# Kernel tuning notes

Hardware: AMD Instinct MI355X
Metric: run time of the kernel (lower is better)

The kernel has to match this reference:

```python
import jax, jax.numpy as jnp
import numpy as np

N_NODES = 100_000
N_EDGES = 1_600_000
N_GRAPHS = 512
NF = 64        # n_node_feats
H1 = 128       # hidden width
H2 = 64        # dim_node_emb
DIM_OUT = 1
STEPS = 4      # set2set processing steps


def _lin(x, W, b):
    # torch Linear convention: y = x @ W.T + b, W: [out, in]
    return x @ W.T + b


def _gelu(x):
    return jax.nn.gelu(x, approximate=False)  # torch.nn.GELU default (erf)


def _lstm_cell(x, h, c, Wih, Whh, bih, bhh):
    g = x @ Wih.T + bih + h @ Whh.T + bhh
    i, f, gg, o = jnp.split(g, 4, axis=-1)  # torch gate order: i, f, g, o
    i, f, o = jax.nn.sigmoid(i), jax.nn.sigmoid(f), jax.nn.sigmoid(o)
    gg = jnp.tanh(gg)
    c = f * c + i * gg
    h = o * jnp.tanh(c)
    return h, c


def setup_inputs() -> dict:
    key = jax.random.key(0)
    ks = jax.random.split(key, 24)
    p = lambda k, shp: jax.random.normal(k, shp, dtype=jnp.float32) * 0.05
    inp = {
        "x": jax.random.normal(ks[0], (N_NODES, NF), dtype=jnp.float32),
        "edge_index": jax.random.randint(ks[1], (2, N_EDGES), 0, N_NODES, dtype=jnp.int32),
        "batch": jnp.sort(jax.random.randint(ks[2], (N_NODES,), 0, N_GRAPHS, dtype=jnp.int32)),
        "nfc_W": p(ks[3], (H1, NF)), "nfc_b": p(ks[4], (H1,)),
        "gc1_W": p(ks[5], (H1, H1)), "gc1_b": p(ks[6], (H1,)),
        "gc2_W": p(ks[7], (H2, H1)), "gc2_b": p(ks[8], (H2,)),
        "lstm0_Wih": p(ks[9], (4 * H2, 2 * H2)), "lstm0_Whh": p(ks[10], (4 * H2, H2)),
        "lstm0_bih": p(ks[11], (4 * H2,)), "lstm0_bhh": p(ks[12], (4 * H2,)),
        "lstm1_Wih": p(ks[13], (4 * H2, H2)), "lstm1_Whh": p(ks[14], (4 * H2, H2)),
        "lstm1_bih": p(ks[15], (4 * H2,)), "lstm1_bhh": p(ks[16], (4 * H2,)),
        "fc1_W": p(ks[17], (32, 2 * H2)), "fc1_b": p(ks[18], (32,)),
        "fc2_W": p(ks[19], (DIM_OUT, 32)), "fc2_b": p(ks[20], (DIM_OUT,)),
    }
    return inp


def _forward(x, edge_index, batch, nfc_W, nfc_b, gc1_W, gc1_b, gc2_W, gc2_b,
             lstm0_Wih, lstm0_Whh, lstm0_bih, lstm0_bhh,
             lstm1_Wih, lstm1_Whh, lstm1_bih, lstm1_bhh,
             fc1_W, fc1_b, fc2_W, fc2_b):
    src, dst = edge_index[0], edge_index[1]

    def gin_conv(h, W, b):
        # PyG GINConv, eps=0: lin((1+eps)*x + sum_{j in N(i)} x_j)
        agg = jax.ops.segment_sum(h[src], dst, num_segments=N_NODES)
        return _lin(h + agg, W, b)

    h = _gelu(_lin(x, nfc_W, nfc_b))
    h = _gelu(gin_conv(h, gc1_W, gc1_b))
    h = _gelu(gin_conv(h, gc2_W, gc2_b))
    # F.normalize(p=2, dim=1)
    h = h / jnp.maximum(jnp.linalg.norm(h, axis=1, keepdims=True), 1e-12)

    # Set2Set: 2-layer LSTM, 4 processing steps, scatter-softmax attention
    B = N_GRAPHS
    h0 = jnp.zeros((B, H2), jnp.float32); c0 = jnp.zeros((B, H2), jnp.float32)
    h1 = jnp.zeros((B, H2), jnp.float32); c1 = jnp.zeros((B, H2), jnp.float32)
    q_star = jnp.zeros((B, 2 * H2), jnp.float32)
    for _ in range(STEPS):
        h0, c0 = _lstm_cell(q_star, h0, c0, lstm0_Wih, lstm0_Whh, lstm0_bih, lstm0_bhh)
        h1, c1 = _lstm_cell(h0, h1, c1, lstm1_Wih, lstm1_Whh, lstm1_bih, lstm1_bhh)
        q = h1  # [B, H2]
        e = jnp.sum(h * q[batch], axis=-1, keepdims=True)  # [N, 1]
        m = jax.ops.segment_max(e, batch, num_segments=B)
        ex = jnp.exp(e - m[batch])
        s = jax.ops.segment_sum(ex, batch, num_segments=B)
        a = ex / (s[batch] + 1e-16)
        r = jax.ops.segment_sum(a * h, batch, num_segments=B)  # [B, H2]
        q_star = jnp.concatenate([q, r], axis=-1)

    z = _gelu(_lin(q_star, fc1_W, fc1_b))
    z = _lin(z, fc2_W, fc2_b)
    return z, h


def reference(x, edge_index, batch, nfc_W, nfc_b, gc1_W, gc1_b, gc2_W, gc2_b,
              lstm0_Wih, lstm0_Whh, lstm0_bih, lstm0_bhh,
              lstm1_Wih, lstm1_Whh, lstm1_bih, lstm1_bhh,
              fc1_W, fc1_b, fc2_W, fc2_b):
    return _forward(x, edge_index, batch, nfc_W, nfc_b, gc1_W, gc1_b, gc2_W, gc2_b,
                    lstm0_Wih, lstm0_Whh, lstm0_bih, lstm0_bhh,
                    lstm1_Wih, lstm1_Whh, lstm1_bih, lstm1_bhh,
                    fc1_W, fc1_b, fc2_W, fc2_b)
```

## Files before the change

### kernel.cpp

```cpp
#include <hip/hip_runtime.h>
#include <hip/hip_bf16.h>
#include <math.h>

constexpr int N  = 100000;
constexpr int E  = 1600000;
constexpr int NG = 512;
constexpr int NF = 64;
constexpr int H1 = 128;
constexpr int H2 = 64;

constexpr int BW   = 256;
constexpr int NB   = (N + BW - 1) / BW;
constexpr int CAP  = 4864;
constexpr int CHUNK = 8192;

constexpr int MAXN = 416;
constexpr int RST  = 68;

typedef __attribute__((ext_vector_type(8))) short short8;
typedef __attribute__((ext_vector_type(4))) float f32x4;

__device__ __forceinline__ float gelu_f(float x) {
    return 0.5f * x * (1.0f + erff(x * 0.70710678118654752f));
}
__device__ __forceinline__ float sigmoid_f(float x) {
    return 1.0f / (1.0f + expf(-x));
}
__device__ __forceinline__ float waveAllSum(float v) {
    #pragma unroll
    for (int m = 32; m; m >>= 1) v += __shfl_xor(v, m);
    return v;
}
__device__ __forceinline__ unsigned short f2bf(float x) {
    __hip_bfloat16 b = __float2bfloat16(x);
    return *reinterpret_cast<unsigned short*>(&b);
}
__device__ __forceinline__ float bf2f(unsigned short u) {
    return __uint_as_float(((unsigned int)u) << 16);
}
__device__ __forceinline__ float bf_lo(unsigned int u) { return __uint_as_float(u << 16); }
__device__ __forceinline__ float bf_hi(unsigned int u) { return __uint_as_float(u & 0xffff0000u); }

__device__ __forceinline__ void bfsplit(float v, unsigned short& hi, unsigned short& lo) {
    hi = f2bf(v);
    lo = f2bf(v - bf2f(hi));
}

__global__ __launch_bounds__(256) void bcur_init_kernel(int* __restrict__ bcursor) {
    int b = blockIdx.x * 256 + threadIdx.x;
    if (b < NB) bcursor[b] = b * CAP;
}

__global__ __launch_bounds__(256) void bin_scatter_kernel(const int* __restrict__ ei,
                                                          int* __restrict__ bcursor,
                                                          int2* __restrict__ pairs) {
    __shared__ int hist[NB];
    __shared__ int start_s[NB];
    __shared__ int lcur[NB];
    int tid = threadIdx.x;
    int e0 = blockIdx.x * CHUNK;
    for (int b = tid; b < NB; b += 256) hist[b] = 0;
    __syncthreads();
    #pragma unroll 4
    for (int k = 0; k < CHUNK / 256; ++k) {
        int e = e0 + k * 256 + tid;
        if (e < E) atomicAdd(&hist[ei[E + e] >> 8], 1);
    }
    __syncthreads();
    for (int b = tid; b < NB; b += 256) {
        if (hist[b]) start_s[b] = atomicAdd(&bcursor[b], hist[b]);
        lcur[b] = 0;
    }
    __syncthreads();
    #pragma unroll 4
    for (int k = 0; k < CHUNK / 256; ++k) {
        int e = e0 + k * 256 + tid;
        if (e < E) {
            int d = ei[E + e];
            int s = ei[e];
            int b = d >> 8;
            int pos = start_s[b] + atomicAdd(&lcur[b], 1);
            if (pos < (b + 1) * CAP) pairs[pos] = make_int2(s, d);
        }
    }
}

__global__ __launch_bounds__(256) void csr_bucket_kernel(const int2* __restrict__ pairs,
                                                         const int* __restrict__ bcursor,
                                                         int* __restrict__ srcs,
                                                         int2* __restrict__ nrange) {
    __shared__ int cnt_l[256];
    __shared__ int cur_l[256];
    __shared__ int wt[4];
    int b = blockIdx.x;
    int tid = threadIdx.x;
    int base = b * CAP;
    int cnt = bcursor[b] - base;
    if (cnt > CAP) cnt = CAP;
    cnt_l[tid] = 0;
    __syncthreads();
    for (int i = tid; i < cnt; i += 256) {
        atomicAdd(&cnt_l[pairs[base + i].y & 255], 1);
    }
    __syncthreads();
    int v = cnt_l[tid];
    int lane = tid & 63, w = tid >> 6;
    int incl = v;
    #pragma unroll
    for (int off = 1; off < 64; off <<= 1) {
        int t = __shfl_up(incl, off);
        if (lane >= off) incl += t;
    }
    if (lane == 63) wt[w] = incl;
    __syncthreads();
    int add = 0;
    for (int i = 0; i < w; ++i) add += wt[i];
    int excl = add + incl - v;
    int node = b * 256 + tid;
    if (node < N) {
        nrange[node] = make_int2(base + excl, base + excl + v);
    }
    cur_l[tid] = excl;
    __syncthreads();
    for (int i = tid; i < cnt; i += 256) {
        int2 p = pairs[base + i];
        int d = p.y & 255;
        int pos = atomicAdd(&cur_l[d], 1);
        srcs[base + pos] = p.x;
    }
}

__global__ __launch_bounds__(256) void gstart_kernel(const int* __restrict__ batch, int* __restrict__ gstart) {
    int g = blockIdx.x * 256 + threadIdx.x;
    if (g > NG) return;
    if (g == NG) { gstart[NG] = N; return; }
    int lo = 0, hi = N;
    while (lo < hi) {
        int mid = (lo + hi) >> 1;
        if (batch[mid] < g) lo = mid + 1; else hi = mid;
    }
    gstart[g] = lo;
}

__global__ __launch_bounds__(256) void wt_kernel(const float* __restrict__ Wih0, const float* __restrict__ Whh0,
                                                 const float* __restrict__ bih0, const float* __restrict__ bhh0,
                                                 const float* __restrict__ Wih1, const float* __restrict__ Whh1,
                                                 const float* __restrict__ bih1, const float* __restrict__ bhh1,
                                                 float* __restrict__ WT0, float* __restrict__ WT1,
                                                 float* __restrict__ b0, float* __restrict__ b1) {
    int i = blockIdx.x * 256 + threadIdx.x;
    if (i < 192 * 256) {
        int k = i >> 8, j = i & 255;
        WT0[i] = (k < 128) ? Wih0[j * 128 + k] : Whh0[j * 64 + (k - 128)];
    }
    if (i < 128 * 256) {
        int k = i >> 8, j = i & 255;
        WT1[i] = (k < 64) ? Wih1[j * 64 + k] : Whh1[j * 64 + (k - 64)];
    }
    if (i < 256) { b0[i] = bih0[i] + bhh0[i]; b1[i] = bih1[i] + bhh1[i]; }
}

template <int ID, int OD, int OUT_MODE>
__global__ __launch_bounds__(256) void lin_mfma_kernel(const float* __restrict__ in,
                                                       const float* __restrict__ W,
                                                       const float* __restrict__ bias,
                                                       void* __restrict__ out_v, int nrows) {
    constexpr int KC = 32;
    constexpr int NCH = ID / KC;
    constexpr int AST = 40;
    constexpr int NCT = OD / 16;
    constexpr int LDSU = 2 * 128 * AST + 2 * OD * AST;
    __shared__ __align__(16) unsigned short lds[LDSU];
    unsigned short* Ahi = lds;
    unsigned short* Alo = lds + 128 * AST;
    unsigned short* Whi = lds + 2 * 128 * AST;
    unsigned short* Wlo = lds + 2 * 128 * AST + OD * AST;

    int tid = threadIdx.x;
    int w = tid >> 6, lane = tid & 63;
    int m15 = lane & 15, quad = lane >> 4;
    int nb = blockIdx.x * 128;

    f32x4 acc[2][NCT];
    #pragma unroll
    for (int rt = 0; rt < 2; ++rt)
        #pragma unroll
        for (int ct = 0; ct < NCT; ++ct) acc[rt][ct] = (f32x4)0.f;

    for (int c = 0; c < NCH; ++c) {
        int kb = c * KC;
        #pragma unroll
        for (int it = 0; it < 4; ++it) {
            int f4 = it * 256 + tid;
            int row = f4 >> 3, kq = (f4 & 7) * 4;
            float4 v = make_float4(0.f, 0.f, 0.f, 0.f);
            if (nb + row < nrows) v = *(const float4*)&in[(size_t)(nb + row) * ID + kb + kq];
            unsigned short h0, h1, h2, h3, l0, l1, l2, l3;
            bfsplit(v.x, h0, l0); bfsplit(v.y, h1, l1);
            bfsplit(v.z, h2, l2); bfsplit(v.w, h3, l3);
            uint2 uh, ul;
            uh.x = (unsigned int)h0 | ((unsigned int)h1 << 16);
            uh.y = (unsigned int)h2 | ((unsigned int)h3 << 16);
            ul.x = (unsigned int)l0 | ((unsigned int)l1 << 16);
            ul.y = (unsigned int)l2 | ((unsigned int)l3 << 16);
            *(uint2*)&Ahi[row * AST + kq] = uh;
            *(uint2*)&Alo[row * AST + kq] = ul;
        }
        #pragma unroll
        for (int it = 0; it < OD / 32; ++it) {
            int f4 = it * 256 + tid;
            int o = f4 >> 3, kq = (f4 & 7) * 4;
            float4 v = *(const float4*)&W[(size_t)o * ID + kb + kq];
            unsigned short h0, h1, h2, h3, l0, l1, l2, l3;
            bfsplit(v.x, h0, l0); bfsplit(v.y, h1, l1);
            bfsplit(v.z, h2, l2); bfsplit(v.w, h3, l3);
            uint2 uh, ul;
            uh.x = (unsigned int)h0 | ((unsigned int)h1 << 16);
            uh.y = (unsigned int)h2 | ((unsigned int)h3 << 16);
            ul.x = (unsigned int)l0 | ((unsigned int)l1 << 16);
            ul.y = (unsigned int)l2 | ((unsigned int)l3 << 16);
            *(uint2*)&Whi[o * AST + kq] = uh;
            *(uint2*)&Wlo[o * AST + kq] = ul;
        }
        __syncthreads();

        short8 ah0 = *(const short8*)&Ahi[(w * 32 + m15) * AST + quad * 8];
        short8 ah1 = *(const short8*)&Ahi[(w * 32 + 16 + m15) * AST + quad * 8];
        short8 al0 = *(const short8*)&Alo[(w * 32 + m15) * AST + quad * 8];
        short8 al1 = *(const short8*)&Alo[(w * 32 + 16 + m15) * AST + quad * 8];
        #pragma unroll
        for (int ct = 0; ct < NCT; ++ct) {
            short8 bh = *(const short8*)&Whi[(ct * 16 + m15) * AST + quad * 8];
            short8 bl = *(const short8*)&Wlo[(ct * 16 + m15) * AST + quad * 8];
            acc[0][ct] = __builtin_amdgcn_mfma_f32_16x16x32_bf16(ah0, bh, acc[0][ct], 0, 0, 0);
            acc[0][ct] = __builtin_amdgcn_mfma_f32_16x16x32_bf16(ah0, bl, acc[0][ct], 0, 0, 0);
            acc[0][ct] = __builtin_amdgcn_mfma_f32_16x16x32_bf16(al0, bh, acc[0][ct], 0, 0, 0);
            acc[1][ct] = __builtin_amdgcn_mfma_f32_16x16x32_bf16(ah1, bh, acc[1][ct], 0, 0, 0);
            acc[1][ct] = __builtin_amdgcn_mfma_f32_16x16x32_bf16(ah1, bl, acc[1][ct], 0, 0, 0);
            acc[1][ct] = __builtin_amdgcn_mfma_f32_16x16x32_bf16(al1, bh, acc[1][ct], 0, 0, 0);
        }
        __syncthreads();
    }

    float bcol[NCT];
    #pragma unroll
    for (int ct = 0; ct < NCT; ++ct) bcol[ct] = bias[ct * 16 + m15];

    if (OUT_MODE == 1) {
        constexpr int EPS = OD + 8;
        unsigned short* ep = lds;
        #pragma unroll
        for (int rt = 0; rt < 2; ++rt)
            #pragma unroll
            for (int ct = 0; ct < NCT; ++ct)
                #pragma unroll
                for (int r = 0; r < 4; ++r) {
                    int rl = w * 32 + rt * 16 + quad * 4 + r;
                    float v = gelu_f(acc[rt][ct][r] + bcol[ct]);
                    ep[rl * EPS + ct * 16 + m15] = f2bf(v);
                }
        __syncthreads();
        constexpr int U4 = 128 * OD / 8;
        for (int i = tid; i < U4; i += 256) {
            int row = i / (OD / 8);
            int off = (i % (OD / 8)) * 8;
            int grow = nb + row;
            if (grow < nrows) {
                uint4 v = *(const uint4*)&ep[row * EPS + off];
                *(uint4*)((unsigned short*)out_v + (size_t)grow * OD + off) = v;
            }
        }
    } else {
        float* out = (float*)out_v;
        #pragma unroll
        for (int rt = 0; rt < 2; ++rt) {
            #pragma unroll
            for (int r = 0; r < 4; ++r) {
                float vv[NCT];
                float ss = 0.f;
                #pragma unroll
                for (int ct = 0; ct < NCT; ++ct) {
                    vv[ct] = gelu_f(acc[rt][ct][r] + bcol[ct]);
                    ss += vv[ct] * vv[ct];
                }
                #pragma unroll
                for (int mm = 1; mm < 16; mm <<= 1) ss += __shfl_xor(ss, mm);
                float denom = fmaxf(sqrtf(ss), 1e-12f);
                int grow = nb + w * 32 + rt * 16 + quad * 4 + r;
                if (grow < nrows) {
                    #pragma unroll
                    for (int ct = 0; ct < NCT; ++ct)
                        out[(size_t)grow * OD + ct * 16 + m15] = vv[ct] / denom;
                }
            }
        }
    }
}

__global__ __launch_bounds__(256) void agg_kernel(const uint2* __restrict__ hb2,
                                                  const int2* __restrict__ nrange,
                                                  const int* __restrict__ srcs,
                                                  float4* __restrict__ out4) {
    int wave = threadIdx.x >> 6, lane = threadIdx.x & 63;
    int half = lane >> 5, hl = lane & 31;
    int n = blockIdx.x * 4 + wave;
    if (n >= N) return;
    int2 rng = nrange[n];
    int s0 = rng.x, deg = rng.y - rng.x;
    int m1 = deg < 64 ? deg : 64;
    int pre = (lane < m1) ? srcs[s0 + lane] : 0;
    float a0 = 0.f, a1 = 0.f, a2 = 0.f, a3 = 0.f;
    int t = 0;
    for (; t + 8 <= m1; t += 8) {
        int i0 = __shfl(pre, t + half);
        int i1 = __shfl(pre, t + 2 + half);
        int i2 = __shfl(pre, t + 4 + half);
        int i3 = __shfl(pre, t + 6 + half);
        uint2 u0 = hb2[(size_t)i0 * 32 + hl];
        uint2 u1 = hb2[(size_t)i1 * 32 + hl];
        uint2 u2 = hb2[(size_t)i2 * 32 + hl];
        uint2 u3 = hb2[(size_t)i3 * 32 + hl];
        a0 += bf_lo(u0.x); a1 += bf_hi(u0.x); a2 += bf_lo(u0.y); a3 += bf_hi(u0.y);
        a0 += bf_lo(u1.x); a1 += bf_hi(u1.x); a2 += bf_lo(u1.y); a3 += bf_hi(u1.y);
        a0 += bf_lo(u2.x); a1 += bf_hi(u2.x); a2 += bf_lo(u2.y); a3 += bf_hi(u2.y);
        a0 += bf_lo(u3.x); a1 += bf_hi(u3.x); a2 += bf_lo(u3.y); a3 += bf_hi(u3.y);
    }
    for (; t < m1; t += 2) {
        int idx = t + half;
        int idc = idx < m1 ? idx : 0;
        int s = __shfl(pre, idc);
        if (idx < m1) {
            uint2 u = hb2[(size_t)s * 32 + hl];
            a0 += bf_lo(u.x); a1 += bf_hi(u.x); a2 += bf_lo(u.y); a3 += bf_hi(u.y);
        }
    }
    for (int j = 64 + half; j < deg; j += 2) {
        int s = srcs[s0 + j];
        uint2 u = hb2[(size_t)s * 32 + hl];
        a0 += bf_lo(u.x); a1 += bf_hi(u.x); a2 += bf_lo(u.y); a3 += bf_hi(u.y);
    }
    a0 += __shfl_down(a0, 32);
    a1 += __shfl_down(a1, 32);
    a2 += __shfl_down(a2, 32);
    a3 += __shfl_down(a3, 32);
    if (half == 0) {
        uint2 u = hb2[(size_t)n * 32 + hl];
        a0 += bf_lo(u.x); a1 += bf_hi(u.x); a2 += bf_lo(u.y); a3 += bf_hi(u.y);
        out4[(size_t)n * 32 + hl] = make_float4(a0, a1, a2, a3);
    }
}

__global__ __launch_bounds__(256) void set2set_kernel(const float* __restrict__ hn,
                                                      const int* __restrict__ gstart,
                                                      const float* __restrict__ WT0, const float* __restrict__ b0,
                                                      const float* __restrict__ WT1, const float* __restrict__ b1,
                                                      float* __restrict__ qstar_out) {
    __shared__ __align__(16) unsigned short hL[MAXN * RST];
    __shared__ float av[MAXN];
    __shared__ __align__(16) float xc0[192];
    __shared__ __align__(16) float xc1[128];
    __shared__ __align__(16) float gates[256];
    __shared__ float c0v[H2], c1v[H2];
    __shared__ float red[4];
    __shared__ float rp[4][H2];
    __shared__ float sp[4];

    int g = blockIdx.x;
    int tid = threadIdx.x, w = tid >> 6, lane = tid & 63;
    int s0 = gstart[g], s1 = gstart[g + 1];
    int cnt = s1 - s0;
    int cL = cnt < MAXN ? cnt : MAXN;
    const float* hq = xc1 + 64;

    for (int idx = tid; idx < cL * 16; idx += 256) {
        int n = idx >> 4, p4 = idx & 15;
        float4 v = *(const float4*)&hn[(size_t)(s0 + n) * 64 + p4 * 4];
        uint2 u;
        u.x = (unsigned int)f2bf(v.x) | ((unsigned int)f2bf(v.y) << 16);
        u.y = (unsigned int)f2bf(v.z) | ((unsigned int)f2bf(v.w) << 16);
        *(uint2*)&hL[n * RST + p4 * 4] = u;
    }
    if (tid < 192) xc0[tid] = 0.f;
    if (tid < 128) xc1[tid] = 0.f;
    if (tid < H2) { c0v[tid] = 0.f; c1v[tid] = 0.f; }
    float b0v = b0[tid], b1v = b1[tid];
    __syncthreads();

    for (int step = 0; step < 4; ++step) {
        {
            float a0 = 0.f, a1 = 0.f, a2 = 0.f, a3 = 0.f;
            #pragma unroll 8
            for (int k = 0; k < 192; k += 4) {
                a0 += xc0[k]     * WT0[(k)     * 256 + tid];
                a1 += xc0[k + 1] * WT0[(k + 1) * 256 + tid];
                a2 += xc0[k + 2] * WT0[(k + 2) * 256 + tid];
                a3 += xc0[k + 3] * WT0[(k + 3) * 256 + tid];
            }
            gates[tid] = (a0 + a1) + (a2 + a3) + b0v;
        }
        __syncthreads();
        if (tid < H2) {
            float ii = sigmoid_f(gates[tid]), ff = sigmoid_f(gates[H2 + tid]);
            float gg = tanhf(gates[2 * H2 + tid]), oo = sigmoid_f(gates[3 * H2 + tid]);
            float c = ff * c0v[tid] + ii * gg;
            float h = oo * tanhf(c);
            c0v[tid] = c; xc0[128 + tid] = h; xc1[tid] = h;
        }
        __syncthreads();
        {
            float a0 = 0.f, a1 = 0.f, a2 = 0.f, a3 = 0.f;
            #pragma unroll 8
            for (int k = 0; k < 128; k += 4) {
                a0 += xc1[k]     * WT1[(k)     * 256 + tid];
                a1 += xc1[k + 1] * WT1[(k + 1) * 256 + tid];
                a2 += xc1[k + 2] * WT1[(k + 2) * 256 + tid];
                a3 += xc1[k + 3] * WT1[(k + 3) * 256 + tid];
            }
            gates[tid] = (a0 + a1) + (a2 + a3) + b1v;
        }
        __syncthreads();
        if (tid < H2) {
            float ii = sigmoid_f(gates[tid]), ff = sigmoid_f(gates[H2 + tid]);
            float gg = tanhf(gates[2 * H2 + tid]), oo = sigmoid_f(gates[3 * H2 + tid]);
            float c = ff * c1v[tid] + ii * gg;
            float h = oo * tanhf(c);
            c1v[tid] = c; xc1[64 + tid] = h;
        }
        __syncthreads();

        float lm = -INFINITY;
        for (int i = tid; i < cnt; i += 256) {
            float e = 0.f;
            if (i < MAXN) {
                const uint2* row = (const uint2*)&hL[i * RST];
                #pragma unroll
                for (int p4 = 0; p4 < 16; ++p4) {
                    uint2 u = row[p4];
                    e += bf_lo(u.x) * hq[p4 * 4 + 0];
                    e += bf_hi(u.x) * hq[p4 * 4 + 1];
                    e += bf_lo(u.y) * hq[p4 * 4 + 2];
                    e += bf_hi(u.y) * hq[p4 * 4 + 3];
                }
                av[i] = e;
            } else {
                for (int f = 0; f < 64; ++f) e += hn[(size_t)(s0 + i) * 64 + f] * hq[f];
            }
            lm = fmaxf(lm, e);
        }
        #pragma unroll
        for (int mm = 32; mm; mm >>= 1) lm = fmaxf(lm, __shfl_xor(lm, mm));
        if (lane == 0) red[w] = lm;
        __syncthreads();
        float m = fmaxf(fmaxf(red[0], red[1]), fmaxf(red[2], red[3]));

        float ps = 0.f;
        for (int i = tid; i < cnt; i += 256) {
            float e;
            if (i < MAXN) e = av[i];
            else {
                e = 0.f;
                for (int f = 0; f < 64; ++f) e += hn[(size_t)(s0 + i) * 64 + f] * hq[f];
            }
            float p = expf(e - m);
            ps += p;
            if (i < MAXN) av[i] = p;
        }
        ps = waveAllSum(ps);
        if (lane == 0) sp[w] = ps;
        __syncthreads();
        float s = sp[0] + sp[1] + sp[2] + sp[3];

        float racc = 0.f;
        for (int i = w; i < cL; i += 4) {
            unsigned short hv = hL[i * RST + lane];
            racc += av[i] * bf2f(hv);
        }
        float qf = hq[lane];
        for (int n = MAXN + w; n < cnt; n += 4) {
            float v = hn[(size_t)(s0 + n) * 64 + lane];
            float e = waveAllSum(v * qf);
            float p = expf(e - m);
            racc += p * v;
        }
        rp[w][lane] = racc;
        __syncthreads();
        if (tid < H2) {
            float r = 0.f;
            if (cnt > 0) {
                r = (rp[0][tid] + rp[1][tid] + rp[2][tid] + rp[3][tid]) / (s + 1e-16f);
            }
            xc0[tid] = xc1[64 + tid];
            xc0[H2 + tid] = r;
        }
        __syncthreads();
    }
    if (tid < 2 * H2) qstar_out[g * 2 * H2 + tid] = xc0[tid];
}

__global__ __launch_bounds__(256) void fcout_kernel(const float* __restrict__ q_star,
                                                    const float* __restrict__ W1, const float* __restrict__ b1,
                                                    const float* __restrict__ W2, const float* __restrict__ b2,
                                                    float* __restrict__ z) {
    __shared__ float W1l[32 * 128];
    __shared__ float b1l[32], W2l[32];
    int tid = threadIdx.x;
    for (int i = tid; i < 32 * 128; i += 256) W1l[i] = W1[i];
    if (tid < 32) { b1l[tid] = b1[tid]; W2l[tid] = W2[tid]; }
    __syncthreads();
    int g = blockIdx.x * 256 + tid;
    float acc[32];
    #pragma unroll
    for (int j = 0; j < 32; ++j) acc[j] = b1l[j];
    for (int k = 0; k < 128; ++k) {
        float qv = q_star[g * 128 + k];
        #pragma unroll
        for (int j = 0; j < 32; ++j) acc[j] += qv * W1l[j * 128 + k];
    }
    float zv = b2[0];
    #pragma unroll
    for (int j = 0; j < 32; ++j) zv += gelu_f(acc[j]) * W2l[j];
    z[g] = zv;
}

extern "C" void kernel_launch(void* const* d_in, const int* in_sizes, int n_in,
                              void* d_out, int out_size, void* d_ws, size_t ws_size,
                              hipStream_t stream) {
    const float* x       = (const float*)d_in[0];
    const int*   ei      = (const int*)d_in[1];
    const int*   batch   = (const int*)d_in[2];
    const float* nfc_W   = (const float*)d_in[3];
    const float* nfc_b   = (const float*)d_in[4];
    const float* gc1_W   = (const float*)d_in[5];
    const float* gc1_b   = (const float*)d_in[6];
    const float* gc2_W   = (const float*)d_in[7];
    const float* gc2_b   = (const float*)d_in[8];
    const float* l0_Wih  = (const float*)d_in[9];
    const float* l0_Whh  = (const float*)d_in[10];
    const float* l0_bih  = (const float*)d_in[11];
    const float* l0_bhh  = (const float*)d_in[12];
    const float* l1_Wih  = (const float*)d_in[13];
    const float* l1_Whh  = (const float*)d_in[14];
    const float* l1_bih  = (const float*)d_in[15];
    const float* l1_bhh  = (const float*)d_in[16];
    const float* fc1_W   = (const float*)d_in[17];
    const float* fc1_b   = (const float*)d_in[18];
    const float* fc2_W   = (const float*)d_in[19];
    const float* fc2_b   = (const float*)d_in[20];

    float* out = (float*)d_out;
    float* hn_out = out + NG;

    char* p = (char*)d_ws;
    auto take = [&](size_t bytes) {
        char* r = p;
        p += (bytes + 255) & ~size_t(255);
        return r;
    };
    float*        sbuf  = (float*)take((size_t)N * H1 * 4);
    unsigned int* hbbuf = (unsigned int*)take((size_t)N * H1 * 2);
    int*   srcs   = (int*)take((size_t)NB * CAP * 4);
    int2*  nrange = (int2*)take((size_t)N * 8);
    int*   bcursor= (int*)take((size_t)NB * 4);
    int*   gstart = (int*)take((size_t)(NG + 1) * 4);
    float* qstar  = (float*)take((size_t)NG * 2 * H2 * 4);
    float* WT0    = (float*)take((size_t)192 * 256 * 4);
    float* WT1    = (float*)take((size_t)128 * 256 * 4);
    float* b0     = (float*)take((size_t)256 * 4);
    float* b1     = (float*)take((size_t)256 * 4);

    int2* pairs = (int2*)sbuf;

    bcur_init_kernel<<<(NB + 255) / 256, 256, 0, stream>>>(bcursor);
    bin_scatter_kernel<<<(E + CHUNK - 1) / CHUNK, 256, 0, stream>>>(ei, bcursor, pairs);
    csr_bucket_kernel<<<NB, 256, 0, stream>>>(pairs, bcursor, srcs, nrange);

    gstart_kernel<<<3, 256, 0, stream>>>(batch, gstart);
    wt_kernel<<<192, 256, 0, stream>>>(l0_Wih, l0_Whh, l0_bih, l0_bhh,
                                       l1_Wih, l1_Whh, l1_bih, l1_bhh, WT0, WT1, b0, b1);

    int mfmaGrid = (N + 127) / 128;
    lin_mfma_kernel<NF, H1, 1><<<mfmaGrid, 256, 0, stream>>>(x, nfc_W, nfc_b, hbbuf, N);
    agg_kernel<<<(N + 3) / 4, 256, 0, stream>>>((const uint2*)hbbuf, nrange, srcs, (float4*)sbuf);
    lin_mfma_kernel<H1, H1, 1><<<mfmaGrid, 256, 0, stream>>>(sbuf, gc1_W, gc1_b, hbbuf, N);
    agg_kernel<<<(N + 3) / 4, 256, 0, stream>>>((const uint2*)hbbuf, nrange, srcs, (float4*)sbuf);
    lin_mfma_kernel<H1, H2, 2><<<mfmaGrid, 256, 0, stream>>>(sbuf, gc2_W, gc2_b, hn_out, N);

    set2set_kernel<<<NG, 256, 0, stream>>>(hn_out, gstart, WT0, b0, WT1, b1, qstar);

    fcout_kernel<<<2, 256, 0, stream>>>(qstar, fc1_W, fc1_b, fc2_W, fc2_b, out);
}
```

Baseline: 469.9 us.

## Pack edge pairs, shrink buckets, merge setup kernels, pre-split agg output

```diff
diff --git a/kernel.cpp b/kernel.cpp
--- a/kernel.cpp
+++ b/kernel.cpp
@@ -9,10 +9,10 @@
 constexpr int H1 = 128;
 constexpr int H2 = 64;
 
-constexpr int BW   = 256;
+constexpr int BW   = 128;
 constexpr int NB   = (N + BW - 1) / BW;
-constexpr int CAP  = 4864;
-constexpr int CHUNK = 8192;
+constexpr int CAP  = 2600;
+constexpr int CHUNK = 2048;
 
 constexpr int MAXN = 416;
 constexpr int RST  = 68;
@@ -46,14 +46,41 @@
     lo = f2bf(v - bf2f(hi));
 }
 
-__global__ __launch_bounds__(256) void bcur_init_kernel(int* __restrict__ bcursor) {
-    int b = blockIdx.x * 256 + threadIdx.x;
-    if (b < NB) bcursor[b] = b * CAP;
+__global__ __launch_bounds__(256) void setup_kernel(const int* __restrict__ batch,
+                                                    const float* __restrict__ Wih0, const float* __restrict__ Whh0,
+                                                    const float* __restrict__ bih0, const float* __restrict__ bhh0,
+                                                    const float* __restrict__ Wih1, const float* __restrict__ Whh1,
+                                                    const float* __restrict__ bih1, const float* __restrict__ bhh1,
+                                                    float* __restrict__ WT0, float* __restrict__ WT1,
+                                                    float* __restrict__ b0, float* __restrict__ b1,
+                                                    int* __restrict__ bcursor, int* __restrict__ gstart) {
+    int i = blockIdx.x * 256 + threadIdx.x;
+    if (i < 192 * 256) {
+        int k = i >> 8, j = i & 255;
+        WT0[i] = (k < 128) ? Wih0[j * 128 + k] : Whh0[j * 64 + (k - 128)];
+    }
+    if (i < 128 * 256) {
+        int k = i >> 8, j = i & 255;
+        WT1[i] = (k < 64) ? Wih1[j * 64 + k] : Whh1[j * 64 + (k - 64)];
+    }
+    if (i < 256) { b0[i] = bih0[i] + bhh0[i]; b1[i] = bih1[i] + bhh1[i]; }
+    if (i < NB) bcursor[i] = i * CAP;
+    if (i <= NG) {
+        if (i == NG) gstart[NG] = N;
+        else {
+            int lo = 0, hi = N;
+            while (lo < hi) {
+                int mid = (lo + hi) >> 1;
+                if (batch[mid] < i) lo = mid + 1; else hi = mid;
+            }
+            gstart[i] = lo;
+        }
+    }
 }
 
 __global__ __launch_bounds__(256) void bin_scatter_kernel(const int* __restrict__ ei,
                                                           int* __restrict__ bcursor,
-                                                          int2* __restrict__ pairs) {
+                                                          int* __restrict__ pairs) {
     __shared__ int hist[NB];
     __shared__ int start_s[NB];
     __shared__ int lcur[NB];
@@ -64,7 +91,7 @@
     #pragma unroll 4
     for (int k = 0; k < CHUNK / 256; ++k) {
         int e = e0 + k * 256 + tid;
-        if (e < E) atomicAdd(&hist[ei[E + e] >> 8], 1);
+        if (e < E) atomicAdd(&hist[ei[E + e] >> 7], 1);
     }
     __syncthreads();
     for (int b = tid; b < NB; b += 256) {
@@ -78,90 +105,59 @@
         if (e < E) {
             int d = ei[E + e];
             int s = ei[e];
-            int b = d >> 8;
+            int b = d >> 7;
             int pos = start_s[b] + atomicAdd(&lcur[b], 1);
-            if (pos < (b + 1) * CAP) pairs[pos] = make_int2(s, d);
-        }
-    }
-}
-
-__global__ __launch_bounds__(256) void csr_bucket_kernel(const int2* __restrict__ pairs,
+            if (pos < (b + 1) * CAP) pairs[pos] = (s << 7) | (d & 127);
+        }
+    }
+}
+
+__global__ __launch_bounds__(256) void csr_bucket_kernel(const int* __restrict__ pairs,
                                                          const int* __restrict__ bcursor,
                                                          int* __restrict__ srcs,
                                                          int2* __restrict__ nrange) {
-    __shared__ int cnt_l[256];
-    __shared__ int cur_l[256];
-    __shared__ int wt[4];
+    __shared__ int cnt_l[BW];
+    __shared__ int cur_l[BW];
+    __shared__ int wt[2];
     int b = blockIdx.x;
     int tid = threadIdx.x;
     int base = b * CAP;
     int cnt = bcursor[b] - base;
     if (cnt > CAP) cnt = CAP;
-    cnt_l[tid] = 0;
+    if (tid < BW) cnt_l[tid] = 0;
     __syncthreads();
     for (int i = tid; i < cnt; i += 256) {
-        atomicAdd(&cnt_l[pairs[base + i].y & 255], 1);
-    }
-    __syncthreads();
-    int v = cnt_l[tid];
-    int lane = tid & 63, w = tid >> 6;
-    int incl = v;
-    #pragma unroll
-    for (int off = 1; off < 64; off <<= 1) {
-        int t = __shfl_up(incl, off);
-        if (lane >= off) incl += t;
-    }
-    if (lane == 63) wt[w] = incl;
-    __syncthreads();
-    int add = 0;
-    for (int i = 0; i < w; ++i) add += wt[i];
-    int excl = add + incl - v;
-    int node = b * 256 + tid;
-    if (node < N) {
-        nrange[node] = make_int2(base + excl, base + excl + v);
-    }
-    cur_l[tid] = excl;
+        atomicAdd(&cnt_l[pairs[base + i] & 127], 1);
+    }
+    __syncthreads();
+    if (tid < BW) {
+        int v = cnt_l[tid];
+        int lane = tid & 63, w = tid >> 6;
+        int incl = v;
+        #pragma unroll
+        for (int off = 1; off < 64; off <<= 1) {
+            int t = __shfl_up(incl, off);
+            if (lane >= off) incl += t;
+        }
+        if (lane == 63) wt[w] = incl;
+        __syncthreads();
+        int excl = (w ? wt[0] : 0) + incl - v;
+        int node = b * BW + tid;
+        if (node < N) nrange[node] = make_int2(base + excl, base + excl + v);
+        cur_l[tid] = excl;
+    } else {
+        __syncthreads();
+    }
     __syncthreads();
     for (int i = tid; i < cnt; i += 256) {
-        int2 p = pairs[base + i];
-        int d = p.y & 255;
-        int pos = atomicAdd(&cur_l[d], 1);
-        srcs[base + pos] = p.x;
-    }
-}
-
-__global__ __launch_bounds__(256) void gstart_kernel(const int* __restrict__ batch, int* __restrict__ gstart) {
-    int g = blockIdx.x * 256 + threadIdx.x;
-    if (g > NG) return;
-    if (g == NG) { gstart[NG] = N; return; }
-    int lo = 0, hi = N;
-    while (lo < hi) {
-        int mid = (lo + hi) >> 1;
-        if (batch[mid] < g) lo = mid + 1; else hi = mid;
-    }
-    gstart[g] = lo;
-}
-
-__global__ __launch_bounds__(256) void wt_kernel(const float* __restrict__ Wih0, const float* __restrict__ Whh0,
-                                                 const float* __restrict__ bih0, const float* __restrict__ bhh0,
-                                                 const float* __restrict__ Wih1, const float* __restrict__ Whh1,
-                                                 const float* __restrict__ bih1, const float* __restrict__ bhh1,
-                                                 float* __restrict__ WT0, float* __restrict__ WT1,
-                                                 float* __restrict__ b0, float* __restrict__ b1) {
-    int i = blockIdx.x * 256 + threadIdx.x;
-    if (i < 192 * 256) {
-        int k = i >> 8, j = i & 255;
-        WT0[i] = (k < 128) ? Wih0[j * 128 + k] : Whh0[j * 64 + (k - 128)];
-    }
-    if (i < 128 * 256) {
-        int k = i >> 8, j = i & 255;
-        WT1[i] = (k < 64) ? Wih1[j * 64 + k] : Whh1[j * 64 + (k - 64)];
-    }
-    if (i < 256) { b0[i] = bih0[i] + bhh0[i]; b1[i] = bih1[i] + bhh1[i]; }
-}
-
-template <int ID, int OD, int OUT_MODE>
-__global__ __launch_bounds__(256) void lin_mfma_kernel(const float* __restrict__ in,
+        int p = pairs[base + i];
+        int pos = atomicAdd(&cur_l[p & 127], 1);
+        srcs[base + pos] = p >> 7;
+    }
+}
+
+template <int ID, int OD, int IN_SPLIT, int OUT_MODE>
+__global__ __launch_bounds__(256) void lin_mfma_kernel(const void* __restrict__ in_v,
                                                        const float* __restrict__ W,
                                                        const float* __restrict__ bias,
                                                        void* __restrict__ out_v, int nrows) {
@@ -189,22 +185,36 @@
 
     for (int c = 0; c < NCH; ++c) {
         int kb = c * KC;
-        #pragma unroll
-        for (int it = 0; it < 4; ++it) {
-            int f4 = it * 256 + tid;
-            int row = f4 >> 3, kq = (f4 & 7) * 4;
-            float4 v = make_float4(0.f, 0.f, 0.f, 0.f);
-            if (nb + row < nrows) v = *(const float4*)&in[(size_t)(nb + row) * ID + kb + kq];
-            unsigned short h0, h1, h2, h3, l0, l1, l2, l3;
-            bfsplit(v.x, h0, l0); bfsplit(v.y, h1, l1);
-            bfsplit(v.z, h2, l2); bfsplit(v.w, h3, l3);
-            uint2 uh, ul;
-            uh.x = (unsigned int)h0 | ((unsigned int)h1 << 16);
-            uh.y = (unsigned int)h2 | ((unsigned int)h3 << 16);
-            ul.x = (unsigned int)l0 | ((unsigned int)l1 << 16);
-            ul.y = (unsigned int)l2 | ((unsigned int)l3 << 16);
-            *(uint2*)&Ahi[row * AST + kq] = uh;
-            *(uint2*)&Alo[row * AST + kq] = ul;
+        if (IN_SPLIT == 0) {
+            const float* in = (const float*)in_v;
+            #pragma unroll
+            for (int it = 0; it < 4; ++it) {
+                int f4 = it * 256 + tid;
+                int row = f4 >> 3, kq = (f4 & 7) * 4;
+                float4 v = make_float4(0.f, 0.f, 0.f, 0.f);
+                if (nb + row < nrows) v = *(const float4*)&in[(size_t)(nb + row) * ID + kb + kq];
+                unsigned short h0, h1, h2, h3, l0, l1, l2, l3;
+                bfsplit(v.x, h0, l0); bfsplit(v.y, h1, l1);
+                bfsplit(v.z, h2, l2); bfsplit(v.w, h3, l3);
+                uint2 uh, ul;
+                uh.x = (unsigned int)h0 | ((unsigned int)h1 << 16);
+                uh.y = (unsigned int)h2 | ((unsigned int)h3 << 16);
+                ul.x = (unsigned int)l0 | ((unsigned int)l1 << 16);
+                ul.y = (unsigned int)l2 | ((unsigned int)l3 << 16);
+                *(uint2*)&Ahi[row * AST + kq] = uh;
+                *(uint2*)&Alo[row * AST + kq] = ul;
+            }
+        } else {
+            const uint4* in4 = (const uint4*)in_v;
+            #pragma unroll
+            for (int it = 0; it < 4; ++it) {
+                int i = it * 256 + tid;
+                int row = i >> 3, grp = i & 7;
+                uint4 u = make_uint4(0u, 0u, 0u, 0u);
+                if (nb + row < nrows) u = in4[(size_t)(nb + row) * 32 + c * 8 + grp];
+                *(uint2*)&Ahi[row * AST + grp * 4] = make_uint2(u.x, u.y);
+                *(uint2*)&Alo[row * AST + grp * 4] = make_uint2(u.z, u.w);
+            }
         }
         #pragma unroll
         for (int it = 0; it < OD / 32; ++it) {
@@ -300,7 +310,7 @@
 __global__ __launch_bounds__(256) void agg_kernel(const uint2* __restrict__ hb2,
                                                   const int2* __restrict__ nrange,
                                                   const int* __restrict__ srcs,
-                                                  float4* __restrict__ out4) {
+                                                  uint4* __restrict__ utab) {
     int wave = threadIdx.x >> 6, lane = threadIdx.x & 63;
     int half = lane >> 5, hl = lane & 31;
     int n = blockIdx.x * 4 + wave;
@@ -346,7 +356,15 @@
     if (half == 0) {
         uint2 u = hb2[(size_t)n * 32 + hl];
         a0 += bf_lo(u.x); a1 += bf_hi(u.x); a2 += bf_lo(u.y); a3 += bf_hi(u.y);
-        out4[(size_t)n * 32 + hl] = make_float4(a0, a1, a2, a3);
+        unsigned short h0, h1, h2, h3, l0, l1, l2, l3;
+        bfsplit(a0, h0, l0); bfsplit(a1, h1, l1);
+        bfsplit(a2, h2, l2); bfsplit(a3, h3, l3);
+        uint4 o;
+        o.x = (unsigned int)h0 | ((unsigned int)h1 << 16);
+        o.y = (unsigned int)h2 | ((unsigned int)h3 << 16);
+        o.z = (unsigned int)l0 | ((unsigned int)l1 << 16);
+        o.w = (unsigned int)l2 | ((unsigned int)l3 << 16);
+        utab[(size_t)n * 32 + hl] = o;
     }
 }
 
@@ -568,22 +586,21 @@
     float* b0     = (float*)take((size_t)256 * 4);
     float* b1     = (float*)take((size_t)256 * 4);
 
-    int2* pairs = (int2*)sbuf;
-
-    bcur_init_kernel<<<(NB + 255) / 256, 256, 0, stream>>>(bcursor);
+    int* pairs = (int*)sbuf;
+
+    setup_kernel<<<192, 256, 0, stream>>>(batch, l0_Wih, l0_Whh, l0_bih, l0_bhh,
+                                          l1_Wih, l1_Whh, l1_bih, l1_bhh,
+                                          WT0, WT1, b0, b1, bcursor, gstart);
+
     bin_scatter_kernel<<<(E + CHUNK - 1) / CHUNK, 256, 0, stream>>>(ei, bcursor, pairs);
     csr_bucket_kernel<<<NB, 256, 0, stream>>>(pairs, bcursor, srcs, nrange);
 
-    gstart_kernel<<<3, 256, 0, stream>>>(batch, gstart);
-    wt_kernel<<<192, 256, 0, stream>>>(l0_Wih, l0_Whh, l0_bih, l0_bhh,
-                                       l1_Wih, l1_Whh, l1_bih, l1_bhh, WT0, WT1, b0, b1);
-
     int mfmaGrid = (N + 127) / 128;
-    lin_mfma_kernel<NF, H1, 1><<<mfmaGrid, 256, 0, stream>>>(x, nfc_W, nfc_b, hbbuf, N);
-    agg_kernel<<<(N + 3) / 4, 256, 0, stream>>>((const uint2*)hbbuf, nrange, srcs, (float4*)sbuf);
-    lin_mfma_kernel<H1, H1, 1><<<mfmaGrid, 256, 0, stream>>>(sbuf, gc1_W, gc1_b, hbbuf, N);
-    agg_kernel<<<(N + 3) / 4, 256, 0, stream>>>((const uint2*)hbbuf, nrange, srcs, (float4*)sbuf);
-    lin_mfma_kernel<H1, H2, 2><<<mfmaGrid, 256, 0, stream>>>(sbuf, gc2_W, gc2_b, hn_out, N);
+    lin_mfma_kernel<NF, H1, 0, 1><<<mfmaGrid, 256, 0, stream>>>(x, nfc_W, nfc_b, hbbuf, N);
+    agg_kernel<<<(N + 3) / 4, 256, 0, stream>>>((const uint2*)hbbuf, nrange, srcs, (uint4*)sbuf);
+    lin_mfma_kernel<H1, H1, 1, 1><<<mfmaGrid, 256, 0, stream>>>(sbuf, gc1_W, gc1_b, hbbuf, N);
+    agg_kernel<<<(N + 3) / 4, 256, 0, stream>>>((const uint2*)hbbuf, nrange, srcs, (uint4*)sbuf);
+    lin_mfma_kernel<H1, H2, 1, 2><<<mfmaGrid, 256, 0, stream>>>(sbuf, gc2_W, gc2_b, hn_out, N);
 
     set2set_kernel<<<NG, 256, 0, stream>>>(hn_out, gstart, WT0, b0, WT1, b1, qstar);
 
```

Result: no change. 474.6 us (+1.0%).
